# Kernel tuning notes

Hardware: AMD Instinct MI355X
Metric: run time of the kernel (lower is better)

## Reference

```python
import jax, jax.numpy as jnp
import numpy as np

N = 50000       # nodes
E_RAND = 800000 # random edges (avg degree 16); self loops appended
IN, HID, H, OUT = 256, 64, 4, 256
NEG_SLOPE = 0.2


def setup_inputs() -> dict:
    key = jax.random.key(0)
    ks = jax.random.split(key, 8)
    x = jax.random.normal(ks[0], (N, IN), dtype=jnp.float32)
    er = jax.random.randint(ks[1], (2, E_RAND), 0, N, dtype=jnp.int32)
    loops = jnp.arange(N, dtype=jnp.int32)
    edge_index = jnp.concatenate([er, jnp.stack([loops, loops])], axis=1)  # [2, E_RAND+N]
    # xavier-ish scaled params
    W1 = jax.random.normal(ks[2], (H * HID, IN), jnp.float32) * (2.0 / (IN + H * HID)) ** 0.5
    a1_src = jax.random.normal(ks[3], (H, HID), jnp.float32) * 0.1
    a1_dst = jax.random.normal(ks[4], (H, HID), jnp.float32) * 0.1
    W2 = jax.random.normal(ks[5], (OUT, H * HID), jnp.float32) * (2.0 / (H * HID + OUT)) ** 0.5
    a2_src = jax.random.normal(ks[6], (1, OUT), jnp.float32) * 0.1
    a2_dst = jax.random.normal(ks[7], (1, OUT), jnp.float32) * 0.1
    return {"x": x, "edge_index": edge_index, "W1": W1, "a1_src": a1_src,
            "a1_dst": a1_dst, "W2": W2, "a2_src": a2_src, "a2_dst": a2_dst}


def gat_layer(h, W, a_src, a_dst, src, dst, concat):
    n = h.shape[0]
    nh, nf = a_src.shape
    hp = (h @ W.T).reshape(n, nh, nf)                 # [N,H,F]
    e = (hp[src] * a_src).sum(-1) + (hp[dst] * a_dst).sum(-1)  # [E,H]
    e = jnp.where(e > 0, e, NEG_SLOPE * e)            # leaky_relu
    e_max = jax.ops.segment_max(e, dst, num_segments=n)
    ex = jnp.exp(e - e_max[dst])
    e_sum = jax.ops.segment_sum(ex, dst, num_segments=n)
    alpha = ex / (e_sum[dst] + 1e-16)                 # [E,H]
    out = jax.ops.segment_sum(hp[src] * alpha[..., None], dst, num_segments=n)
    return out.reshape(n, nh * nf) if concat else out.mean(axis=1)


def reference(x, edge_index, W1, a1_src, a1_dst, W2, a2_src, a2_dst):
    src, dst = edge_index[0], edge_index[1]
    h = jax.nn.relu(gat_layer(x, W1, a1_src, a1_dst, src, dst, True))
    return gat_layer(h, W2, a2_src, a2_dst, src, dst, False)
```

## Files before the change

### kernel.cpp

```cpp
#include <hip/hip_runtime.h>
#include <math.h>


typedef __attribute__((ext_vector_type(8))) short short8;
typedef __attribute__((ext_vector_type(8))) unsigned short ushort8;
typedef __attribute__((ext_vector_type(4))) float f32x4;
typedef _Float16 half8 __attribute__((ext_vector_type(8)));

__device__ inline unsigned short f2h(float f) {
    _Float16 h = (_Float16)f;
    unsigned short u;
    __builtin_memcpy(&u, &h, 2);
    return u;
}
__device__ inline float h2f(unsigned short u) {
    _Float16 h;
    __builtin_memcpy(&h, &u, 2);
    return (float)h;
}

__global__ void convert_h8(const float* __restrict__ X, unsigned short* __restrict__ Xh,
                           long n) {
    long i = ((long)blockIdx.x * 256 + threadIdx.x) * 8;
    if (i + 8 <= n) {
        float4 v0 = *(const float4*)&X[i];
        float4 v1 = *(const float4*)&X[i + 4];
        ushort8 o;
        o[0] = f2h(v0.x); o[1] = f2h(v0.y); o[2] = f2h(v0.z); o[3] = f2h(v0.w);
        o[4] = f2h(v1.x); o[5] = f2h(v1.y); o[6] = f2h(v1.z); o[7] = f2h(v1.w);
        *(ushort8*)&Xh[i] = o;
    } else {
        for (long k = i; k < n; ++k) Xh[k] = f2h(X[k]);
    }
}

__global__ void convert_w2(const float* __restrict__ WA, const float* __restrict__ WB,
                           unsigned short* __restrict__ DA, unsigned short* __restrict__ DB) {
    const bool second = blockIdx.x >= 32;
    const float* S = second ? WB : WA;
    unsigned short* D = second ? DB : DA;
    long i = ((long)(blockIdx.x & 31) * 256 + threadIdx.x) * 8;
    float4 v0 = *(const float4*)&S[i];
    float4 v1 = *(const float4*)&S[i + 4];
    ushort8 o;
    o[0] = f2h(v0.x); o[1] = f2h(v0.y); o[2] = f2h(v0.z); o[3] = f2h(v0.w);
    o[4] = f2h(v1.x); o[5] = f2h(v1.y); o[6] = f2h(v1.z); o[7] = f2h(v1.w);
    *(ushort8*)&D[i] = o;
}

__global__ __launch_bounds__(256) void gemm_mfma(const unsigned short* __restrict__ A_g,
                                                 const unsigned short* __restrict__ B_g,
                                                 unsigned short* __restrict__ C, int M) {
    __shared__ unsigned short Ah[128 * 40];
    __shared__ unsigned short Bh[128 * 40];
    const int tid = threadIdx.x;
    const int m0 = blockIdx.x * 128;
    const int n0 = blockIdx.y * 128;
    const int w = tid >> 6, lane = tid & 63;
    const int l15 = lane & 15, q = lane >> 4;

    f32x4 acc[2][8];
    #pragma unroll
    for (int mt = 0; mt < 2; ++mt)
        #pragma unroll
        for (int nt = 0; nt < 8; ++nt) acc[mt][nt] = (f32x4){0.f, 0.f, 0.f, 0.f};

    const int ar = tid >> 1;
    const int ak = (tid & 1) * 16;

    for (int k0 = 0; k0 < 256; k0 += 32) {
        int gm = m0 + ar;
        if (gm < M) {
            const unsigned short* a0 = &A_g[(size_t)gm * 256 + k0 + ak];
            *(ushort8*)&Ah[ar * 40 + ak]     = *(const ushort8*)a0;
            *(ushort8*)&Ah[ar * 40 + ak + 8] = *(const ushort8*)(a0 + 8);
        } else {
            ushort8 z = (ushort8){0, 0, 0, 0, 0, 0, 0, 0};
            *(ushort8*)&Ah[ar * 40 + ak]     = z;
            *(ushort8*)&Ah[ar * 40 + ak + 8] = z;
        }
        {
            const unsigned short* b0 = &B_g[(size_t)(n0 + ar) * 256 + k0 + ak];
            *(ushort8*)&Bh[ar * 40 + ak]     = *(const ushort8*)b0;
            *(ushort8*)&Bh[ar * 40 + ak + 8] = *(const ushort8*)(b0 + 8);
        }
        __syncthreads();
        half8 a[2];
        #pragma unroll
        for (int mt = 0; mt < 2; ++mt) {
            int rowA = w * 32 + mt * 16 + l15;
            a[mt] = *(half8*)&Ah[rowA * 40 + q * 8];
        }
        #pragma unroll
        for (int nt = 0; nt < 8; ++nt) {
            int rowB = nt * 16 + l15;
            half8 bf = *(half8*)&Bh[rowB * 40 + q * 8];
            #pragma unroll
            for (int mt = 0; mt < 2; ++mt)
                acc[mt][nt] = __builtin_amdgcn_mfma_f32_16x16x32_f16(a[mt], bf, acc[mt][nt], 0, 0, 0);
        }
        __syncthreads();
    }
    #pragma unroll
    for (int mt = 0; mt < 2; ++mt) {
        #pragma unroll
        for (int nt = 0; nt < 8; ++nt) {
            #pragma unroll
            for (int r = 0; r < 4; ++r) {
                int gm = m0 + w * 32 + mt * 16 + q * 4 + r;
                if (gm < M) C[(size_t)gm * 256 + n0 + nt * 16 + l15] = f2h(acc[mt][nt][r]);
            }
        }
    }
}

__global__ void zero_int(int* __restrict__ p, int n) {
    int i = blockIdx.x * 256 + threadIdx.x;
    if (i < n) p[i] = 0;
}

__global__ void hist_kernel(const int* __restrict__ dst, int* __restrict__ deg, int E) {
    int i = blockIdx.x * 256 + threadIdx.x;
    if (i < E) atomicAdd(&deg[dst[i]], 1);
}

__global__ __launch_bounds__(1024) void scan1(const int* __restrict__ deg,
                                              int* __restrict__ lex,
                                              int* __restrict__ bsums, int n) {
    __shared__ int sh[1024];
    int tid = threadIdx.x;
    int i = blockIdx.x * 1024 + tid;
    int v = (i < n) ? deg[i] : 0;
    sh[tid] = v;
    __syncthreads();
    #pragma unroll
    for (int off = 1; off < 1024; off <<= 1) {
        int t2 = (tid >= off) ? sh[tid - off] : 0;
        __syncthreads();
        sh[tid] += t2;
        __syncthreads();
    }
    if (i < n) lex[i] = sh[tid] - v;
    if (tid == 1023) bsums[blockIdx.x] = sh[1023];
}

__global__ __launch_bounds__(1024) void scan23(int* __restrict__ offs,
                                               int* __restrict__ cur,
                                               const int* __restrict__ bsums,
                                               int n, int nb) {
    __shared__ int s_boff, s_total;
    int tid = threadIdx.x;
    if (tid < 64) {
        int bv = (tid < nb) ? bsums[tid] : 0;
        int v = bv;
        #pragma unroll
        for (int off = 1; off < 64; off <<= 1) {
            int t = __shfl_up(v, off, 64);
            if (tid >= off) v += t;
        }
        int incl_bid = __shfl(v, blockIdx.x, 64);
        int bv_bid   = __shfl(bv, blockIdx.x, 64);
        int total    = __shfl(v, nb - 1, 64);
        if (tid == 0) {
            s_boff = incl_bid - bv_bid;
            s_total = total;
        }
    }
    __syncthreads();
    int i = blockIdx.x * 1024 + tid;
    if (i < n) {
        int o = offs[i] + s_boff;
        offs[i] = o;
        cur[i] = o;
    }
    if (blockIdx.x == 0 && tid == 0) offs[n] = s_total;
}

__global__ void scatter_kernel(const int* __restrict__ src, const int* __restrict__ dst,
                               int* __restrict__ cur, int* __restrict__ sorted, int E) {
    int i = blockIdx.x * 256 + threadIdx.x;
    if (i < E) {
        int p = atomicAdd(&cur[dst[i]], 1);
        sorted[p] = src[i];
    }
}

__global__ __launch_bounds__(256) void sort_csr(const int* __restrict__ offs,
                                                int* __restrict__ sorted, int N) {
    const int w = threadIdx.x >> 6, lane = threadIdx.x & 63;
    const int node = blockIdx.x * 4 + w;
    if (node >= N) return;
    const int b = offs[node], e = offs[node + 1];
    const int deg = e - b;
    if (deg < 2 || deg > 64) return;
    int key = (lane < deg) ? sorted[b + lane] : 0x7FFFFFFF;
    #pragma unroll
    for (int k = 2; k <= 64; k <<= 1) {
        #pragma unroll
        for (int j = k >> 1; j > 0; j >>= 1) {
            int other = __shfl_xor(key, j, 64);
            bool keepMin = ((lane & j) == 0) == ((lane & k) == 0);
            int mn = min(key, other), mh = max(key, other);
            key = keepMin ? mn : mh;
        }
    }
    if (lane < deg) sorted[b + lane] = key;
}

template <int NH>
__global__ __launch_bounds__(256) void scompute(const unsigned short* __restrict__ hp,
                                                const float* __restrict__ a_src,
                                                const float* __restrict__ a_dst,
                                                float* __restrict__ s_src,
                                                float* __restrict__ s_dst, int N) {
    const int w = threadIdx.x >> 6, lane = threadIdx.x & 63;
    const int node = blockIdx.x * 4 + w;
    if (node >= N) return;
    const int f0 = lane * 4;
    ushort4 uv = *(const ushort4*)(hp + (size_t)node * 256 + f0);
    float4 as = *(const float4*)(a_src + f0);
    float4 ad = *(const float4*)(a_dst + f0);
    float x0 = h2f(uv.x), x1 = h2f(uv.y), x2 = h2f(uv.z), x3 = h2f(uv.w);
    float p1 = x0 * as.x + x1 * as.y + x2 * as.z + x3 * as.w;
    float p2 = x0 * ad.x + x1 * ad.y + x2 * ad.z + x3 * ad.w;
    if constexpr (NH == 4) {
        #pragma unroll
        for (int off = 1; off < 16; off <<= 1) {
            p1 += __shfl_xor(p1, off, 64);
            p2 += __shfl_xor(p2, off, 64);
        }
        if ((lane & 15) == 0) {
            s_src[node * 4 + (lane >> 4)] = p1;
            s_dst[node * 4 + (lane >> 4)] = p2;
        }
    } else {
        #pragma unroll
        for (int off = 1; off < 64; off <<= 1) {
            p1 += __shfl_xor(p1, off, 64);
            p2 += __shfl_xor(p2, off, 64);
        }
        if (lane == 0) {
            s_src[node] = p1;
            s_dst[node] = p2;
        }
    }
}

template <int NH, bool RELU, bool F16OUT>
__global__ __launch_bounds__(256) void aggregate4(const unsigned short* __restrict__ hp,
                                                  const float* __restrict__ ssrc,
                                                  const float* __restrict__ sdst,
                                                  const int* __restrict__ offs,
                                                  const int* __restrict__ sorted,
                                                  float* __restrict__ out,
                                                  unsigned short* __restrict__ outh, int N) {
    __shared__ int   s_sh[4][64];
    __shared__ float p_sh[4][64][NH];

    const int w = threadIdx.x >> 6, lane = threadIdx.x & 63;
    const int node_raw = blockIdx.x * 4 + w;
    const bool node_ok = node_raw < N;
    const int node = node_ok ? node_raw : (N - 1);
    constexpr int NF = 256 / NH;

    const int b = offs[node], e = offs[node + 1];
    const int deg = e - b;

    float sv[NH];
    #pragma unroll
    for (int h = 0; h < NH; ++h) sv[h] = sdst[node * NH + h];

    float lv[NH], mx[NH];
    const bool small = (deg <= 64);

    if (small) {
        const bool valid = lane < deg;
        const int mys = valid ? sorted[b + lane] : 0;

        float evv[NH];
        if constexpr (NH == 4) {
            float4 sa = *(const float4*)&ssrc[(size_t)mys * 4];
            evv[0] = sa.x + sv[0]; evv[1] = sa.y + sv[1];
            evv[2] = sa.z + sv[2]; evv[3] = sa.w + sv[3];
        } else {
            evv[0] = ssrc[mys] + sv[0];
        }
        #pragma unroll
        for (int h = 0; h < NH; ++h) {
            float ev = evv[h];
            ev = ev > 0.f ? ev : 0.2f * ev;
            evv[h] = valid ? ev : -INFINITY;
            mx[h] = evv[h];
        }
        #pragma unroll
        for (int off = 32; off > 0; off >>= 1)
            #pragma unroll
            for (int h = 0; h < NH; ++h)
                mx[h] = fmaxf(mx[h], __shfl_xor(mx[h], off, 64));

        float pv[NH];
        #pragma unroll
        for (int h = 0; h < NH; ++h) {
            pv[h] = valid ? __expf(evv[h] - mx[h]) : 0.f;
            lv[h] = pv[h];
        }
        #pragma unroll
        for (int off = 32; off > 0; off >>= 1)
            #pragma unroll
            for (int h = 0; h < NH; ++h)
                lv[h] += __shfl_xor(lv[h], off, 64);

        s_sh[w][lane] = mys;
        #pragma unroll
        for (int h = 0; h < NH; ++h) p_sh[w][lane][h] = pv[h];
    } else {
        #pragma unroll
        for (int h = 0; h < NH; ++h) mx[h] = -INFINITY;
        for (int c = b + lane; c < e; c += 64) {
            int s = sorted[c];
            #pragma unroll
            for (int h = 0; h < NH; ++h) {
                float ev = ssrc[s * NH + h] + sv[h];
                ev = ev > 0.f ? ev : 0.2f * ev;
                mx[h] = fmaxf(mx[h], ev);
            }
        }
        #pragma unroll
        for (int off = 32; off > 0; off >>= 1)
            #pragma unroll
            for (int h = 0; h < NH; ++h)
                mx[h] = fmaxf(mx[h], __shfl_xor(mx[h], off, 64));
    }

    __syncthreads();

    if (small) {
        const int quarter = lane >> 4;
        const int l16 = lane & 15;
        const int f0 = l16 * 16;
        const int head = f0 / NF;

        float acc[16];
        #pragma unroll
        for (int k = 0; k < 16; ++k) acc[k] = 0.f;

        const int iters = (deg + 3) >> 2;
        int t2 = 0;
        for (; t2 + 2 <= iters; t2 += 2) {
            int j0 = 4 * t2 + quarter;
            int j1 = j0 + 4;
            bool ok0 = j0 < deg, ok1 = j1 < deg;
            int jj0 = ok0 ? j0 : 0, jj1 = ok1 ? j1 : 0;
            int s0 = s_sh[w][jj0];
            int s1 = s_sh[w][jj1];
            float p0 = ok0 ? p_sh[w][jj0][head] : 0.f;
            float p1 = ok1 ? p_sh[w][jj1][head] : 0.f;
            const unsigned short* r0 = hp + (size_t)s0 * 256 + f0;
            const unsigned short* r1 = hp + (size_t)s1 * 256 + f0;
            half8 va0 = *(const half8*)(r0);
            half8 va1 = *(const half8*)(r0 + 8);
            half8 vb0 = *(const half8*)(r1);
            half8 vb1 = *(const half8*)(r1 + 8);
            #pragma unroll
            for (int k = 0; k < 8; ++k) {
                acc[k]     = fmaf(p0, (float)va0[k], acc[k]);
                acc[8 + k] = fmaf(p0, (float)va1[k], acc[8 + k]);
            }
            #pragma unroll
            for (int k = 0; k < 8; ++k) {
                acc[k]     = fmaf(p1, (float)vb0[k], acc[k]);
                acc[8 + k] = fmaf(p1, (float)vb1[k], acc[8 + k]);
            }
        }
        if (t2 < iters) {
            int j = 4 * t2 + quarter;
            bool jv = j < deg;
            int jj = jv ? j : 0;
            int s = s_sh[w][jj];
            float p = jv ? p_sh[w][jj][head] : 0.f;
            const unsigned short* row = hp + (size_t)s * 256 + f0;
            half8 v0 = *(const half8*)(row);
            half8 v1 = *(const half8*)(row + 8);
            #pragma unroll
            for (int k = 0; k < 8; ++k) {
                acc[k]     = fmaf(p, (float)v0[k], acc[k]);
                acc[8 + k] = fmaf(p, (float)v1[k], acc[8 + k]);
            }
        }
        #pragma unroll
        for (int k = 0; k < 16; ++k) {
            acc[k] += __shfl_xor(acc[k], 16, 64);
            acc[k] += __shfl_xor(acc[k], 32, 64);
        }
        if (node_ok && lane < 16) {
            float li = 1.0f / (lv[head] + 1e-16f);
            float o[16];
            #pragma unroll
            for (int k = 0; k < 16; ++k) {
                o[k] = acc[k] * li;
                if (RELU) o[k] = fmaxf(o[k], 0.f);
            }
            if constexpr (F16OUT) {
                ushort8 u0, u1;
                #pragma unroll
                for (int k = 0; k < 8; ++k) {
                    u0[k] = f2h(o[k]);
                    u1[k] = f2h(o[8 + k]);
                }
                *(ushort8*)&outh[(size_t)node * 256 + f0]     = u0;
                *(ushort8*)&outh[(size_t)node * 256 + f0 + 8] = u1;
            } else {
                float* op = &out[(size_t)node * 256 + f0];
                *(float4*)&op[0]  = make_float4(o[0], o[1], o[2], o[3]);
                *(float4*)&op[4]  = make_float4(o[4], o[5], o[6], o[7]);
                *(float4*)&op[8]  = make_float4(o[8], o[9], o[10], o[11]);
                *(float4*)&op[12] = make_float4(o[12], o[13], o[14], o[15]);
            }
        }
    } else {
        const int half = lane >> 5;
        const int l32 = lane & 31;
        const int f0 = l32 * 8;
        const int head = f0 / NF;

        float acc[8];
        #pragma unroll
        for (int k = 0; k < 8; ++k) acc[k] = 0.f;
        #pragma unroll
        for (int h = 0; h < NH; ++h) lv[h] = 0.f;

        int last = -1, round = 0;
        for (;;) {
            int myMin = 0x7FFFFFFF, myCnt = 0;
            for (int c = b + lane; c < e; c += 64) {
                int s = sorted[c];
                if (s > last) {
                    if (s < myMin) { myMin = s; myCnt = 1; }
                    else if (s == myMin) ++myCnt;
                }
            }
            #pragma unroll
            for (int off = 32; off > 0; off >>= 1) {
                int om = __shfl_xor(myMin, off, 64);
                int oc = __shfl_xor(myCnt, off, 64);
                if (om < myMin) { myMin = om; myCnt = oc; }
                else if (om == myMin) myCnt += oc;
            }
            if (myMin == 0x7FFFFFFF) break;
            const bool mine = ((round & 1) == half);
            float cf = (float)myCnt;
            float ph[NH];
            #pragma unroll
            for (int h = 0; h < NH; ++h) {
                float ev = ssrc[myMin * NH + h] + sv[h];
                ev = ev > 0.f ? ev : 0.2f * ev;
                ph[h] = __expf(ev - mx[h]);
            }
            if (mine && l32 == 0) {
                #pragma unroll
                for (int h = 0; h < NH; ++h) lv[h] += cf * ph[h];
            }
            if (mine) {
                float p = cf * ph[head];
                half8 v = *(const half8*)(hp + (size_t)myMin * 256 + f0);
                #pragma unroll
                for (int k = 0; k < 8; ++k) acc[k] = fmaf(p, (float)v[k], acc[k]);
            }
            last = myMin; ++round;
        }
        #pragma unroll
        for (int off = 32; off > 0; off >>= 1)
            #pragma unroll
            for (int h = 0; h < NH; ++h)
                lv[h] += __shfl_xor(lv[h], off, 64);

        #pragma unroll
        for (int k = 0; k < 8; ++k) acc[k] += __shfl_xor(acc[k], 32, 64);

        if (node_ok && lane < 32) {
            float li = 1.0f / (lv[head] + 1e-16f);
            float o[8];
            #pragma unroll
            for (int k = 0; k < 8; ++k) {
                o[k] = acc[k] * li;
                if (RELU) o[k] = fmaxf(o[k], 0.f);
            }
            if constexpr (F16OUT) {
                ushort8 u0;
                #pragma unroll
                for (int k = 0; k < 8; ++k) u0[k] = f2h(o[k]);
                *(ushort8*)&outh[(size_t)node * 256 + f0] = u0;
            } else {
                *(float4*)&out[(size_t)node * 256 + f0]     = make_float4(o[0], o[1], o[2], o[3]);
                *(float4*)&out[(size_t)node * 256 + f0 + 4] = make_float4(o[4], o[5], o[6], o[7]);
            }
        }
    }
}

extern "C" void kernel_launch(void* const* d_in, const int* in_sizes, int n_in,
                              void* d_out, int out_size, void* d_ws, size_t ws_size,
                              hipStream_t stream) {
    const float* x   = (const float*)d_in[0];
    const int*   ei  = (const int*)d_in[1];
    const float* W1  = (const float*)d_in[2];
    const float* a1s = (const float*)d_in[3];
    const float* a1d = (const float*)d_in[4];
    const float* W2  = (const float*)d_in[5];
    const float* a2s = (const float*)d_in[6];
    const float* a2d = (const float*)d_in[7];
    float* out = (float*)d_out;

    const int N = in_sizes[0] / 256;
    const int E = in_sizes[1] / 2;
    const int* src = ei;
    const int* dst = ei + E;

    unsigned short* hp = (unsigned short*)d_ws;
    float* ssrc  = (float*)(hp + (size_t)N * 256);
    float* sdst  = ssrc + (size_t)N * 4;
    int*   deg   = (int*)(sdst + (size_t)N * 4);
    int*   cur   = deg + N;
    int*   offs  = cur + N;
    int*   sorted= offs + N + 1;
    int*   bsums = sorted + E;
    int*   boffs = bsums + 64;
    unsigned short* w1h = (unsigned short*)(boffs + 64);
    unsigned short* w2h = w1h + 65536;

    unsigned short* xh = (unsigned short*)d_out;
    unsigned short* hh = xh + (size_t)N * 256;

    const int nb = (N + 1023) / 1024;

    convert_w2<<<64, 256, 0, stream>>>(W1, W2, w1h, w2h);
    long nx = (long)N * 256;
    convert_h8<<<(int)((nx / 8 + 255) / 256), 256, 0, stream>>>(x, xh, nx);

    zero_int<<<(N + 255) / 256, 256, 0, stream>>>(deg, N);
    hist_kernel<<<(E + 255) / 256, 256, 0, stream>>>(dst, deg, E);
    scan1<<<nb, 1024, 0, stream>>>(deg, offs, bsums, N);
    scan23<<<nb, 1024, 0, stream>>>(offs, cur, bsums, N, nb);
    scatter_kernel<<<(E + 255) / 256, 256, 0, stream>>>(src, dst, cur, sorted, E);

    dim3 gg((N + 127) / 128, 2);
    int aggblocks = (N + 3) / 4;
    sort_csr<<<aggblocks, 256, 0, stream>>>(offs, sorted, N);

    gemm_mfma<<<gg, 256, 0, stream>>>(xh, w1h, hp, N);
    scompute<4><<<aggblocks, 256, 0, stream>>>(hp, a1s, a1d, ssrc, sdst, N);
    aggregate4<4, true, true><<<aggblocks, 256, 0, stream>>>(hp, ssrc, sdst, offs, sorted,
                                                             nullptr, hh, N);

    gemm_mfma<<<gg, 256, 0, stream>>>(hh, w2h, hp, N);
    scompute<1><<<aggblocks, 256, 0, stream>>>(hp, a2s, a2d, ssrc, sdst, N);
    aggregate4<1, false, false><<<aggblocks, 256, 0, stream>>>(hp, ssrc, sdst, offs, sorted,
                                                               out, nullptr, N);
}
```

Before: 421.2 us.

## Fuse fp32-to-fp16 input conversion into GEMM and use full-width N tiles

```diff
diff --git a/kernel.cpp b/kernel.cpp
--- a/kernel.cpp
+++ b/kernel.cpp
@@ -17,21 +17,6 @@
     _Float16 h;
     __builtin_memcpy(&h, &u, 2);
     return (float)h;
-}
-
-__global__ void convert_h8(const float* __restrict__ X, unsigned short* __restrict__ Xh,
-                           long n) {
-    long i = ((long)blockIdx.x * 256 + threadIdx.x) * 8;
-    if (i + 8 <= n) {
-        float4 v0 = *(const float4*)&X[i];
-        float4 v1 = *(const float4*)&X[i + 4];
-        ushort8 o;
-        o[0] = f2h(v0.x); o[1] = f2h(v0.y); o[2] = f2h(v0.z); o[3] = f2h(v0.w);
-        o[4] = f2h(v1.x); o[5] = f2h(v1.y); o[6] = f2h(v1.z); o[7] = f2h(v1.w);
-        *(ushort8*)&Xh[i] = o;
-    } else {
-        for (long k = i; k < n; ++k) Xh[k] = f2h(X[k]);
-    }
 }
 
 __global__ void convert_w2(const float* __restrict__ WA, const float* __restrict__ WB,
@@ -48,68 +33,69 @@
     *(ushort8*)&D[i] = o;
 }
 
-__global__ __launch_bounds__(256) void gemm_mfma(const unsigned short* __restrict__ A_g,
+template <bool AF32>
+__global__ __launch_bounds__(256) void gemm_mfma(const void* __restrict__ A_gv,
                                                  const unsigned short* __restrict__ B_g,
                                                  unsigned short* __restrict__ C, int M) {
-    __shared__ unsigned short Ah[128 * 40];
-    __shared__ unsigned short Bh[128 * 40];
+    __shared__ unsigned short Ah[64 * 40];
+    __shared__ unsigned short Bh[256 * 40];
     const int tid = threadIdx.x;
-    const int m0 = blockIdx.x * 128;
-    const int n0 = blockIdx.y * 128;
+    const int m0 = blockIdx.x * 64;
     const int w = tid >> 6, lane = tid & 63;
     const int l15 = lane & 15, q = lane >> 4;
 
-    f32x4 acc[2][8];
+    f32x4 acc[16];
     #pragma unroll
-    for (int mt = 0; mt < 2; ++mt)
-        #pragma unroll
-        for (int nt = 0; nt < 8; ++nt) acc[mt][nt] = (f32x4){0.f, 0.f, 0.f, 0.f};
-
-    const int ar = tid >> 1;
-    const int ak = (tid & 1) * 16;
+    for (int nt = 0; nt < 16; ++nt) acc[nt] = (f32x4){0.f, 0.f, 0.f, 0.f};
+
+    const int ar = tid >> 2;
+    const int ak = (tid & 3) * 8;
 
     for (int k0 = 0; k0 < 256; k0 += 32) {
         int gm = m0 + ar;
+        ushort8 aval;
         if (gm < M) {
-            const unsigned short* a0 = &A_g[(size_t)gm * 256 + k0 + ak];
-            *(ushort8*)&Ah[ar * 40 + ak]     = *(const ushort8*)a0;
-            *(ushort8*)&Ah[ar * 40 + ak + 8] = *(const ushort8*)(a0 + 8);
+            if constexpr (AF32) {
+                const float* A_g = (const float*)A_gv;
+                const float* ap = &A_g[(size_t)gm * 256 + k0 + ak];
+                float4 v0 = *(const float4*)(ap);
+                float4 v1 = *(const float4*)(ap + 4);
+                aval[0] = f2h(v0.x); aval[1] = f2h(v0.y);
+                aval[2] = f2h(v0.z); aval[3] = f2h(v0.w);
+                aval[4] = f2h(v1.x); aval[5] = f2h(v1.y);
+                aval[6] = f2h(v1.z); aval[7] = f2h(v1.w);
+            } else {
+                const unsigned short* A_g = (const unsigned short*)A_gv;
+                aval = *(const ushort8*)&A_g[(size_t)gm * 256 + k0 + ak];
+            }
         } else {
-            ushort8 z = (ushort8){0, 0, 0, 0, 0, 0, 0, 0};
-            *(ushort8*)&Ah[ar * 40 + ak]     = z;
-            *(ushort8*)&Ah[ar * 40 + ak + 8] = z;
-        }
+            aval = (ushort8){0, 0, 0, 0, 0, 0, 0, 0};
+        }
+        *(ushort8*)&Ah[ar * 40 + ak] = aval;
         {
-            const unsigned short* b0 = &B_g[(size_t)(n0 + ar) * 256 + k0 + ak];
-            *(ushort8*)&Bh[ar * 40 + ak]     = *(const ushort8*)b0;
-            *(ushort8*)&Bh[ar * 40 + ak + 8] = *(const ushort8*)(b0 + 8);
+            const unsigned short* b0 = &B_g[(size_t)tid * 256 + k0];
+            *(ushort8*)&Bh[tid * 40 + 0]  = *(const ushort8*)(b0);
+            *(ushort8*)&Bh[tid * 40 + 8]  = *(const ushort8*)(b0 + 8);
+            *(ushort8*)&Bh[tid * 40 + 16] = *(const ushort8*)(b0 + 16);
+            *(ushort8*)&Bh[tid * 40 + 24] = *(const ushort8*)(b0 + 24);
         }
         __syncthreads();
-        half8 a[2];
-        #pragma unroll
-        for (int mt = 0; mt < 2; ++mt) {
-            int rowA = w * 32 + mt * 16 + l15;
-            a[mt] = *(half8*)&Ah[rowA * 40 + q * 8];
-        }
-        #pragma unroll
-        for (int nt = 0; nt < 8; ++nt) {
+        int rowA = w * 16 + l15;
+        half8 a = *(half8*)&Ah[rowA * 40 + q * 8];
+        #pragma unroll
+        for (int nt = 0; nt < 16; ++nt) {
             int rowB = nt * 16 + l15;
             half8 bf = *(half8*)&Bh[rowB * 40 + q * 8];
-            #pragma unroll
-            for (int mt = 0; mt < 2; ++mt)
-                acc[mt][nt] = __builtin_amdgcn_mfma_f32_16x16x32_f16(a[mt], bf, acc[mt][nt], 0, 0, 0);
+            acc[nt] = __builtin_amdgcn_mfma_f32_16x16x32_f16(a, bf, acc[nt], 0, 0, 0);
         }
         __syncthreads();
     }
     #pragma unroll
-    for (int mt = 0; mt < 2; ++mt) {
-        #pragma unroll
-        for (int nt = 0; nt < 8; ++nt) {
-            #pragma unroll
-            for (int r = 0; r < 4; ++r) {
-                int gm = m0 + w * 32 + mt * 16 + q * 4 + r;
-                if (gm < M) C[(size_t)gm * 256 + n0 + nt * 16 + l15] = f2h(acc[mt][nt][r]);
-            }
+    for (int nt = 0; nt < 16; ++nt) {
+        #pragma unroll
+        for (int r = 0; r < 4; ++r) {
+            int gm = m0 + w * 16 + q * 4 + r;
+            if (gm < M) C[(size_t)gm * 256 + nt * 16 + l15] = f2h(acc[nt][r]);
         }
     }
 }
@@ -345,34 +331,7 @@
         for (int k = 0; k < 16; ++k) acc[k] = 0.f;
 
         const int iters = (deg + 3) >> 2;
-        int t2 = 0;
-        for (; t2 + 2 <= iters; t2 += 2) {
-            int j0 = 4 * t2 + quarter;
-            int j1 = j0 + 4;
-            bool ok0 = j0 < deg, ok1 = j1 < deg;
-            int jj0 = ok0 ? j0 : 0, jj1 = ok1 ? j1 : 0;
-            int s0 = s_sh[w][jj0];
-            int s1 = s_sh[w][jj1];
-            float p0 = ok0 ? p_sh[w][jj0][head] : 0.f;
-            float p1 = ok1 ? p_sh[w][jj1][head] : 0.f;
-            const unsigned short* r0 = hp + (size_t)s0 * 256 + f0;
-            const unsigned short* r1 = hp + (size_t)s1 * 256 + f0;
-            half8 va0 = *(const half8*)(r0);
-            half8 va1 = *(const half8*)(r0 + 8);
-            half8 vb0 = *(const half8*)(r1);
-            half8 vb1 = *(const half8*)(r1 + 8);
-            #pragma unroll
-            for (int k = 0; k < 8; ++k) {
-                acc[k]     = fmaf(p0, (float)va0[k], acc[k]);
-                acc[8 + k] = fmaf(p0, (float)va1[k], acc[8 + k]);
-            }
-            #pragma unroll
-            for (int k = 0; k < 8; ++k) {
-                acc[k]     = fmaf(p1, (float)vb0[k], acc[k]);
-                acc[8 + k] = fmaf(p1, (float)vb1[k], acc[8 + k]);
-            }
-        }
-        if (t2 < iters) {
+        for (int t2 = 0; t2 < iters; ++t2) {
             int j = 4 * t2 + quarter;
             bool jv = j < deg;
             int jj = jv ? j : 0;
@@ -528,14 +487,11 @@
     unsigned short* w1h = (unsigned short*)(boffs + 64);
     unsigned short* w2h = w1h + 65536;
 
-    unsigned short* xh = (unsigned short*)d_out;
-    unsigned short* hh = xh + (size_t)N * 256;
+    unsigned short* hh = (unsigned short*)d_out;
 
     const int nb = (N + 1023) / 1024;
 
     convert_w2<<<64, 256, 0, stream>>>(W1, W2, w1h, w2h);
-    long nx = (long)N * 256;
-    convert_h8<<<(int)((nx / 8 + 255) / 256), 256, 0, stream>>>(x, xh, nx);
 
     zero_int<<<(N + 255) / 256, 256, 0, stream>>>(deg, N);
     hist_kernel<<<(E + 255) / 256, 256, 0, stream>>>(dst, deg, E);
@@ -543,16 +499,16 @@
     scan23<<<nb, 1024, 0, stream>>>(offs, cur, bsums, N, nb);
     scatter_kernel<<<(E + 255) / 256, 256, 0, stream>>>(src, dst, cur, sorted, E);
 
-    dim3 gg((N + 127) / 128, 2);
+    int gemmblocks = (N + 63) / 64;
     int aggblocks = (N + 3) / 4;
     sort_csr<<<aggblocks, 256, 0, stream>>>(offs, sorted, N);
 
-    gemm_mfma<<<gg, 256, 0, stream>>>(xh, w1h, hp, N);
+    gemm_mfma<true><<<gemmblocks, 256, 0, stream>>>(x, w1h, hp, N);
     scompute<4><<<aggblocks, 256, 0, stream>>>(hp, a1s, a1d, ssrc, sdst, N);
     aggregate4<4, true, true><<<aggblocks, 256, 0, stream>>>(hp, ssrc, sdst, offs, sorted,
                                                              nullptr, hh, N);
 
-    gemm_mfma<<<gg, 256, 0, stream>>>(hh, w2h, hp, N);
+    gemm_mfma<false><<<gemmblocks, 256, 0, stream>>>(hh, w2h, hp, N);
     scompute<1><<<aggblocks, 256, 0, stream>>>(hp, a2s, a2d, ssrc, sdst, N);
     aggregate4<1, false, false><<<aggblocks, 256, 0, stream>>>(hp, ssrc, sdst, offs, sorted,
                                                                out, nullptr, N);
```

After: 415.1 us. About the same (-1.5%).
